# Optimization experiments

Measured on AMD Instinct MI355X. Metric: run time of the kernel, lower is better.

## Reference

```python
import jax, jax.numpy as jnp
import numpy as np

HIDDEN = 1024
D_INNER = 2048      # expand * hidden
STATE = 16          # state_dim n
DT_RANK = 64        # ceil(hidden/16)
D_CONV = 4
B, S = 2, 2048
EPS = 1e-5


def setup_inputs() -> dict:
    key = jax.random.key(0)
    ks = jax.random.split(key, 10)
    sc = lambda fan_in: 1.0 / np.sqrt(fan_in)
    x = jax.random.normal(ks[0], (B, S, HIDDEN), dtype=jnp.float32)
    norm_w = jnp.ones((HIDDEN,), dtype=jnp.float32)
    in_proj_w = jax.random.uniform(ks[1], (2 * D_INNER, HIDDEN), minval=-sc(HIDDEN), maxval=sc(HIDDEN), dtype=jnp.float32)
    conv_w = jax.random.uniform(ks[2], (D_INNER, 1, D_CONV), minval=-sc(D_CONV), maxval=sc(D_CONV), dtype=jnp.float32)
    conv_b = jax.random.uniform(ks[3], (D_INNER,), minval=-sc(D_CONV), maxval=sc(D_CONV), dtype=jnp.float32)
    x_proj_w = jax.random.uniform(ks[4], (DT_RANK + 2 * STATE, D_INNER), minval=-sc(D_INNER), maxval=sc(D_INNER), dtype=jnp.float32)
    dt_proj_w = jax.random.uniform(ks[5], (D_INNER, DT_RANK), minval=-sc(DT_RANK), maxval=sc(DT_RANK), dtype=jnp.float32)
    dt_proj_b = jax.random.uniform(ks[6], (D_INNER,), minval=-sc(DT_RANK), maxval=sc(DT_RANK), dtype=jnp.float32)
    A_log = jnp.log(jnp.broadcast_to(jnp.arange(1, STATE + 1, dtype=jnp.float32), (D_INNER, STATE)))
    D = jnp.ones((D_INNER,), dtype=jnp.float32)
    out_proj_w = jax.random.uniform(ks[7], (HIDDEN, D_INNER), minval=-sc(D_INNER), maxval=sc(D_INNER), dtype=jnp.float32)
    return {"x": x, "norm_w": norm_w, "in_proj_w": in_proj_w, "conv_w": conv_w,
            "conv_b": conv_b, "x_proj_w": x_proj_w, "dt_proj_w": dt_proj_w,
            "dt_proj_b": dt_proj_b, "A_log": A_log, "D": D, "out_proj_w": out_proj_w}


def _selective_scan(u, delta, A, Bm, Cm, D):
    # u, delta: [b,s,d]; A: [d,n]; Bm, Cm: [b,s,n]; D: [d]
    deltaA = jnp.exp(jnp.einsum('bsd,dn->bsdn', delta, A))          # [b,s,d,n]
    deltaB_u = jnp.einsum('bsd,bsn,bsd->bsdn', delta, Bm, u)        # [b,s,d,n]

    def step(h, inp):
        dA_t, dBu_t, C_t = inp                                       # [b,d,n],[b,d,n],[b,n]
        h = dA_t * h + dBu_t
        y = jnp.einsum('bdn,bn->bd', h, C_t)
        return h, y

    h0 = jnp.zeros((u.shape[0], u.shape[2], A.shape[1]), dtype=u.dtype)
    _, ys = jax.lax.scan(step, h0,
                         (deltaA.transpose(1, 0, 2, 3),
                          deltaB_u.transpose(1, 0, 2, 3),
                          Cm.transpose(1, 0, 2)))
    y = ys.transpose(1, 0, 2)                                        # [b,s,d]
    return y + u * D


def reference(x, norm_w, in_proj_w, conv_w, conv_b, x_proj_w, dt_proj_w,
              dt_proj_b, A_log, D, out_proj_w):
    # RMSNorm
    xn = x * jax.lax.rsqrt(jnp.mean(x * x, axis=-1, keepdims=True) + EPS) * norm_w

    # in_proj -> split
    x_and_res = xn @ in_proj_w.T                                     # [b,s,2*d_inner]
    xi, res = jnp.split(x_and_res, 2, axis=-1)

    # causal depthwise conv1d (left-pad d_conv-1, truncate to s)
    xc = jax.lax.conv_general_dilated(
        xi.transpose(0, 2, 1), conv_w,
        window_strides=(1,), padding=[(D_CONV - 1, 0)],
        dimension_numbers=('NCH', 'OIH', 'NCH'),
        feature_group_count=D_INNER) + conv_b[None, :, None]
    xc = jax.nn.silu(xc.transpose(0, 2, 1))                          # [b,s,d_inner]

    # ssm
    A = -jnp.exp(A_log)
    x_dbl = xc @ x_proj_w.T                                          # [b,s,dt_rank+2n]
    dt, Bm, Cm = jnp.split(x_dbl, [DT_RANK, DT_RANK + STATE], axis=-1)
    delta = jax.nn.softplus(dt @ dt_proj_w.T + dt_proj_b)            # [b,s,d_inner]
    y = _selective_scan(xc, delta, A, Bm, Cm, D)

    y = y * jax.nn.silu(res)
    out = y @ out_proj_w.T
    return out + x
```

## Files before the change

### kernel.cpp

```cpp
#include <hip/hip_runtime.h>
#include <math.h>

#define HIDDEN   1024
#define D_INNER  2048
#define NSTATE   16
#define DT_RANK  64
#define BATCH    2
#define SEQ      2048
#define T_TOK    (BATCH * SEQ)
#define XDBL     (DT_RANK + 2 * NSTATE)
#define NCH      64
#define CHL      (SEQ / NCH)
#define BDN      (BATCH * D_INNER * NSTATE)

typedef float f32x4   __attribute__((ext_vector_type(4)));
typedef short bf16x8  __attribute__((ext_vector_type(8)));
typedef short short4v __attribute__((ext_vector_type(4)));

#define AS1 __attribute__((address_space(1)))
#define AS3 __attribute__((address_space(3)))
#define GLOAD(src, dst) __builtin_amdgcn_global_load_lds( \
    (const AS1 unsigned int*)(src), (AS3 unsigned int*)(dst), 16, 0, 0)

__device__ __forceinline__ float silu_f(float x) { return x / (1.0f + __expf(-x)); }
__device__ __forceinline__ float softplus_f(float x) {
    return fmaxf(x, 0.0f) + log1pf(__expf(-fabsf(x)));
}
__device__ __forceinline__ unsigned short f2bf(float x) {
    unsigned int u = __float_as_uint(x);
    u += 0x7fffu + ((u >> 16) & 1u);
    return (unsigned short)(u >> 16);
}
__device__ __forceinline__ float bf2f(unsigned short h) {
    return __uint_as_float(((unsigned int)h) << 16);
}

__device__ __forceinline__ void pack_seg(
        const float* __restrict__ w, unsigned short* __restrict__ wp,
        int K, int segs, int i) {
    int kq = K >> 2;
    int row = i / kq;
    int c = (i - row * kq) << 2;
    float4 v = *(const float4*)(w + (size_t)row * K + c);
    short4v hi, lo;
    hi.x = f2bf(v.x); hi.y = f2bf(v.y); hi.z = f2bf(v.z); hi.w = f2bf(v.w);
    lo.x = f2bf(v.x - bf2f(hi.x)); lo.y = f2bf(v.y - bf2f(hi.y));
    lo.z = f2bf(v.z - bf2f(hi.z)); lo.w = f2bf(v.w - bf2f(hi.w));
    size_t b0 = (size_t)row * (segs * K) + c;
    *(short4v*)(wp + b0) = hi;
    if (segs == 2) *(short4v*)(wp + b0 + K) = lo;
}

__global__ __launch_bounds__(256) void wpack_all_kernel(
        const float* __restrict__ win,  unsigned short* __restrict__ pin,
        const float* __restrict__ wout, unsigned short* __restrict__ pout,
        const float* __restrict__ wx,   unsigned short* __restrict__ px,
        const float* __restrict__ wdt,  unsigned short* __restrict__ pdt) {
    int bid = blockIdx.x;
    int t = threadIdx.x;
    if (bid < 4096) {
        pack_seg(win, pin, HIDDEN, 1, bid * 256 + t);
    } else if (bid < 6144) {
        pack_seg(wout, pout, D_INNER, 1, (bid - 4096) * 256 + t);
    } else if (bid < 6336) {
        pack_seg(wx, px, D_INNER, 2, (bid - 6144) * 256 + t);
    } else {
        pack_seg(wdt, pdt, DT_RANK, 2, (bid - 6336) * 256 + t);
    }
}

__global__ __launch_bounds__(256) void rmsnorm_pack_kernel(
        const float* __restrict__ x, const float* __restrict__ w,
        unsigned short* __restrict__ xn_p) {
    int row = blockIdx.x;
    float4 v = ((const float4*)(x + (size_t)row * HIDDEN))[threadIdx.x];
    float ss = v.x*v.x + v.y*v.y + v.z*v.z + v.w*v.w;
    #pragma unroll
    for (int off = 32; off; off >>= 1) ss += __shfl_down(ss, off);
    __shared__ float wsum[4];
    if ((threadIdx.x & 63) == 0) wsum[threadIdx.x >> 6] = ss;
    __syncthreads();
    float scale = rsqrtf((wsum[0] + wsum[1] + wsum[2] + wsum[3]) / (float)HIDDEN + 1e-5f);
    float4 wv = ((const float4*)w)[threadIdx.x];
    float o0 = v.x * scale * wv.x, o1 = v.y * scale * wv.y;
    float o2 = v.z * scale * wv.z, o3 = v.w * scale * wv.w;
    short4v hi, lo;
    hi.x = f2bf(o0); hi.y = f2bf(o1); hi.z = f2bf(o2); hi.w = f2bf(o3);
    lo.x = f2bf(o0 - bf2f(hi.x)); lo.y = f2bf(o1 - bf2f(hi.y));
    lo.z = f2bf(o2 - bf2f(hi.z)); lo.w = f2bf(o3 - bf2f(hi.w));
    size_t b0 = (size_t)row * (2 * HIDDEN) + threadIdx.x * 4;
    *(short4v*)&xn_p[b0]          = hi;
    *(short4v*)&xn_p[b0 + HIDDEN] = lo;
}

template<int EPI>
__global__ __launch_bounds__(256, 2) void mgemm2_kernel(
        const unsigned short* __restrict__ Ap, int Asr, int loOff,
        const unsigned short* __restrict__ Wp, int Wsr,
        int klen, float* __restrict__ C0, float* __restrict__ C1,
        int ldout, size_t partStride) {
    __shared__ short Ah[128 * 64];
    __shared__ short Al[128 * 64];
    __shared__ short Bh[256 * 64];
    const int t = threadIdx.x;
    const int w = t >> 6, l = t & 63;
    const int m0 = blockIdx.y * 128, n0 = blockIdx.x * 256;
    const int kbeg = blockIdx.z * klen;
    const int lrow = l & 15;
    f32x4 acc[8][4];
    #pragma unroll
    for (int m = 0; m < 8; ++m)
        #pragma unroll
        for (int n = 0; n < 4; ++n) {
            acc[m][n].x = 0.f; acc[m][n].y = 0.f; acc[m][n].z = 0.f; acc[m][n].w = 0.f;
        }
    const int srow8 = l >> 3;
    const int sc8   = (l & 7) ^ srow8;
    const unsigned short* ga = Ap + (size_t)(m0 + w * 32 + srow8) * Asr + sc8 * 8;
    const unsigned short* gb = Wp + (size_t)(n0 + w * 64 + srow8) * Wsr + sc8 * 8;
    for (int k0 = kbeg; k0 < kbeg + klen; k0 += 64) {
        __syncthreads();
        #pragma unroll
        for (int q = 0; q < 4; ++q) {
            const int ar = (w * 32 + q * 8) * 128;
            GLOAD(ga + k0 + (size_t)q * 8 * Asr,         (char*)Ah + ar);
            GLOAD(ga + loOff + k0 + (size_t)q * 8 * Asr, (char*)Al + ar);
        }
        #pragma unroll
        for (int q = 0; q < 8; ++q)
            GLOAD(gb + k0 + (size_t)q * 8 * Wsr, (char*)Bh + (w * 64 + q * 8) * 128);
        __syncthreads();
        #pragma unroll
        for (int kk = 0; kk < 2; ++kk) {
            const int slot = ((kk * 4 + (l >> 4)) ^ (l & 7)) * 8;
            bf16x8 bh[4];
            #pragma unroll
            for (int n = 0; n < 4; ++n)
                bh[n] = *(const bf16x8*)&Bh[(w * 64 + n * 16 + lrow) * 64 + slot];
            #pragma unroll
            for (int m = 0; m < 8; ++m) {
                bf16x8 ah = *(const bf16x8*)&Ah[(m * 16 + lrow) * 64 + slot];
                bf16x8 al = *(const bf16x8*)&Al[(m * 16 + lrow) * 64 + slot];
                #pragma unroll
                for (int n = 0; n < 4; ++n) {
                    acc[m][n] = __builtin_amdgcn_mfma_f32_16x16x32_bf16(
                        ah, bh[n], acc[m][n], 0, 0, 0);
                    acc[m][n] = __builtin_amdgcn_mfma_f32_16x16x32_bf16(
                        al, bh[n], acc[m][n], 0, 0, 0);
                }
            }
        }
    }
    float* dst;
    int cbase;
    if (EPI == 0) {
        dst   = (n0 < D_INNER) ? C0 : C1;
        cbase = (n0 < D_INNER) ? n0 : n0 - D_INNER;
    } else {
        dst   = C0 + blockIdx.z * partStride;
        cbase = n0;
    }
    #pragma unroll
    for (int m = 0; m < 8; ++m) {
        #pragma unroll
        for (int n = 0; n < 4; ++n) {
            #pragma unroll
            for (int j = 0; j < 4; ++j) {
                int row = m0 + m * 16 + (l >> 4) * 4 + j;
                int col = cbase + w * 64 + n * 16 + (l & 15);
                dst[(size_t)row * ldout + col] = acc[m][n][j];
            }
        }
    }
}

template<int EPI>
__global__ __launch_bounds__(256) void mgemm_kernel(
        const unsigned short* __restrict__ Ap, const unsigned short* __restrict__ Wp,
        int Klog, int klen, int brows, float* __restrict__ C0,
        int ldout, size_t partStride, const float* __restrict__ bias) {
    __shared__ short lds[4 * 128 * 64];
    short* Ah = lds;
    short* Al = lds + 128 * 64;
    short* Bh = lds + 2 * 128 * 64;
    short* Bl = lds + 3 * 128 * 64;
    const int t = threadIdx.x;
    const int w = t >> 6, l = t & 63;
    const int m0 = blockIdx.y * 128, n0 = blockIdx.x * 128;
    const int kbeg = blockIdx.z * klen;
    const int wr = (w >> 1) * 64, wc = (w & 1) * 64;
    const int lrow = l & 15;
    f32x4 acc[4][4];
    #pragma unroll
    for (int m = 0; m < 4; ++m)
        #pragma unroll
        for (int n = 0; n < 4; ++n) {
            acc[m][n].x = 0.f; acc[m][n].y = 0.f; acc[m][n].z = 0.f; acc[m][n].w = 0.f;
        }
    const int Asr = 2 * Klog;
    const int Wsr = 2 * Klog;
    const int srow = w * 32 + (l >> 3);
    const int sc8  = (l & 7) ^ ((l >> 3) & 7);
    const int brow = min(n0 + srow, brows - 1);
    const unsigned short* ga = Ap + (size_t)(m0 + srow) * Asr + sc8 * 8;
    const unsigned short* gb = Wp + (size_t)brow * Wsr + sc8 * 8;
    for (int k0 = kbeg; k0 < kbeg + klen; k0 += 64) {
        __syncthreads();
        #pragma unroll
        for (int q = 0; q < 4; ++q) {
            const int doff = (w * 32 + q * 8) * 128;
            GLOAD(ga + k0 + (size_t)q * 8 * Asr,        (char*)Ah + doff);
            GLOAD(ga + Klog + k0 + (size_t)q * 8 * Asr, (char*)Al + doff);
            GLOAD(gb + k0 + (size_t)q * 8 * Wsr,        (char*)Bh + doff);
            GLOAD(gb + Klog + k0 + (size_t)q * 8 * Wsr, (char*)Bl + doff);
        }
        __syncthreads();
        #pragma unroll
        for (int kk = 0; kk < 2; ++kk) {
            const int slot = ((kk * 4 + (l >> 4)) ^ (l & 7)) * 8;
            bf16x8 ah[4], al[4], bh[4], bl[4];
            #pragma unroll
            for (int m = 0; m < 4; ++m) {
                ah[m] = *(const bf16x8*)&Ah[(wr + m * 16 + lrow) * 64 + slot];
                al[m] = *(const bf16x8*)&Al[(wr + m * 16 + lrow) * 64 + slot];
            }
            #pragma unroll
            for (int n = 0; n < 4; ++n) {
                bh[n] = *(const bf16x8*)&Bh[(wc + n * 16 + lrow) * 64 + slot];
                bl[n] = *(const bf16x8*)&Bl[(wc + n * 16 + lrow) * 64 + slot];
            }
            #pragma unroll
            for (int m = 0; m < 4; ++m)
                #pragma unroll
                for (int n = 0; n < 4; ++n) {
                    acc[m][n] = __builtin_amdgcn_mfma_f32_16x16x32_bf16(
                        ah[m], bh[n], acc[m][n], 0, 0, 0);
                    acc[m][n] = __builtin_amdgcn_mfma_f32_16x16x32_bf16(
                        al[m], bh[n], acc[m][n], 0, 0, 0);
                    acc[m][n] = __builtin_amdgcn_mfma_f32_16x16x32_bf16(
                        ah[m], bl[n], acc[m][n], 0, 0, 0);
                }
        }
    }
    float* dst = (EPI == 2) ? (C0 + blockIdx.z * partStride) : C0;
    #pragma unroll
    for (int m = 0; m < 4; ++m) {
        #pragma unroll
        for (int n = 0; n < 4; ++n) {
            #pragma unroll
            for (int j = 0; j < 4; ++j) {
                int row = m0 + wr + m * 16 + (l >> 4) * 4 + j;
                int col = n0 + wc + n * 16 + (l & 15);
                float v = acc[m][n][j];
                if (EPI == 2) {
                    dst[(size_t)row * ldout + col] = v;
                } else {
                    C0[(size_t)row * ldout + col] = softplus_f(v + bias[col]);
                }
            }
        }
    }
}

__global__ __launch_bounds__(256) void reduce4_kernel(
        const float* __restrict__ parts, size_t partStride,
        const float* __restrict__ x, float* __restrict__ out) {
    size_t i = (size_t)blockIdx.x * 256 + threadIdx.x;
    float4 a = ((const float4*)(parts))[i];
    float4 b = ((const float4*)(parts + partStride))[i];
    float4 c = ((const float4*)(parts + 2 * partStride))[i];
    float4 d = ((const float4*)(parts + 3 * partStride))[i];
    float4 xv = ((const float4*)x)[i];
    float4 o;
    o.x = a.x + b.x + c.x + d.x + xv.x;
    o.y = a.y + b.y + c.y + d.y + xv.y;
    o.z = a.z + b.z + c.z + d.z + xv.z;
    o.w = a.w + b.w + c.w + d.w + xv.w;
    ((float4*)out)[i] = o;
}

__global__ __launch_bounds__(256) void reduceX_kernel(
        const float* __restrict__ parts, float* __restrict__ xdbl,
        unsigned short* __restrict__ dtp) {
    int i = blockIdx.x * 256 + threadIdx.x;
    int row = i / 24;
    int c = (i - row * 24) * 4;
    float4 s = make_float4(0.f, 0.f, 0.f, 0.f);
    #pragma unroll
    for (int z = 0; z < 8; ++z) {
        float4 a = *(const float4*)(parts + (size_t)z * 524288 + (size_t)row * 128 + c);
        s.x += a.x; s.y += a.y; s.z += a.z; s.w += a.w;
    }
    *(float4*)(xdbl + (size_t)row * XDBL + c) = s;
    if (c < DT_RANK) {
        short4v hi, lo;
        hi.x = f2bf(s.x); hi.y = f2bf(s.y); hi.z = f2bf(s.z); hi.w = f2bf(s.w);
        lo.x = f2bf(s.x - bf2f(hi.x)); lo.y = f2bf(s.y - bf2f(hi.y));
        lo.z = f2bf(s.z - bf2f(hi.z)); lo.w = f2bf(s.w - bf2f(hi.w));
        size_t b0 = (size_t)row * 128 + c;
        *(short4v*)(dtp + b0)      = hi;
        *(short4v*)(dtp + b0 + 64) = lo;
    }
}

__global__ __launch_bounds__(256) void conv_silu_kernel(
        const float* __restrict__ xi, const float* __restrict__ w,
        const float* __restrict__ b, unsigned short* __restrict__ xc_p) {
    size_t i = (size_t)blockIdx.x * 256 + threadIdx.x;
    int d = (int)(i & (D_INNER - 1));
    int tt = (int)(i >> 11);
    int s = tt & (SEQ - 1);
    float4 wv = ((const float4*)w)[d];
    float acc = b[d];
    if (s >= 3) acc += wv.x * xi[i - 3 * D_INNER];
    if (s >= 2) acc += wv.y * xi[i - 2 * D_INNER];
    if (s >= 1) acc += wv.z * xi[i - 1 * D_INNER];
    acc += wv.w * xi[i];
    float o = silu_f(acc);
    unsigned short hi = f2bf(o);
    unsigned short lo = f2bf(o - bf2f(hi));
    size_t o2 = (size_t)tt * (2 * D_INNER) + d;
    xc_p[o2]           = hi;
    xc_p[o2 + D_INNER] = lo;
}


__global__ __launch_bounds__(256) void scanA_kernel(
        const unsigned short* __restrict__ xcp, const float* __restrict__ delta,
        const float* __restrict__ xdbl, const float* __restrict__ A_log,
        float* __restrict__ hpart, float* __restrict__ Pp) {
    __shared__ float sB[CHL * NSTATE];
    const int bid = blockIdx.x;
    const int b    = bid >> 9;
    const int c    = (bid >> 3) & 63;
    const int dblk = bid & 7;
    const int d    = (dblk << 8) + threadIdx.x;
    const int rowbase = b * SEQ + c * CHL;
    #pragma unroll
    for (int q = 0; q < 2; ++q) {
        int e = threadIdx.x + q * 256;
        int r = e >> 4, n = e & 15;
        sB[e] = xdbl[(size_t)(rowbase + r) * XDBL + DT_RANK + n];
    }
    float adn[NSTATE];
    #pragma unroll
    for (int k = 0; k < 4; ++k) {
        float4 a = *(const float4*)(A_log + d * NSTATE + k * 4);
        adn[k*4+0] = -__expf(a.x); adn[k*4+1] = -__expf(a.y);
        adn[k*4+2] = -__expf(a.z); adn[k*4+3] = -__expf(a.w);
    }
    float h[NSTATE], P[NSTATE];
    #pragma unroll
    for (int n = 0; n < NSTATE; ++n) { h[n] = 0.f; P[n] = 1.f; }
    __syncthreads();
    #pragma unroll 4
    for (int r = 0; r < CHL; ++r) {
        const int row = rowbase + r;
        const float* brow = &sB[r * NSTATE];
        size_t o2 = (size_t)row * (2 * D_INNER) + d;
        float dl = delta[(size_t)row * D_INNER + d];
        float u  = bf2f(xcp[o2]) + bf2f(xcp[o2 + D_INNER]);
        float du = dl * u;
        #pragma unroll
        for (int n = 0; n < NSTATE; ++n) {
            float dA = __expf(dl * adn[n]);
            h[n] = fmaf(dA, h[n], du * brow[n]);
            P[n] *= dA;
        }
    }
    size_t base = (size_t)c * BDN + (size_t)(b * D_INNER + d) * NSTATE;
    #pragma unroll
    for (int k = 0; k < 4; ++k) {
        *(float4*)(hpart + base + k * 4) = make_float4(h[k*4], h[k*4+1], h[k*4+2], h[k*4+3]);
        *(float4*)(Pp    + base + k * 4) = make_float4(P[k*4], P[k*4+1], P[k*4+2], P[k*4+3]);
    }
}

__global__ __launch_bounds__(256) void scanB_kernel(
        float* __restrict__ hpart, const float* __restrict__ Pp) {
    int idx = blockIdx.x * 256 + threadIdx.x;
    float h = 0.f;
    for (int c = 0; c < NCH; ++c) {
        size_t o = (size_t)c * BDN + idx;
        float hp = hpart[o];
        float p  = Pp[o];
        hpart[o] = h;
        h = fmaf(p, h, hp);
    }
}

__global__ __launch_bounds__(256) void scanC_kernel(
        const unsigned short* xcp, const float* __restrict__ delta,
        const float* __restrict__ xdbl, const float* __restrict__ A_log,
        const float* __restrict__ Dp, const float* __restrict__ hstart,
        const float* __restrict__ res, unsigned short* y_p) {
    __shared__ float sB[CHL * NSTATE];
    __shared__ float sC[CHL * NSTATE];
    const int bid = blockIdx.x;
    const int b    = bid >> 9;
    const int c    = (bid >> 3) & 63;
    const int dblk = bid & 7;
    const int d    = (dblk << 8) + threadIdx.x;
    const int rowbase = b * SEQ + c * CHL;
    #pragma unroll
    for (int q = 0; q < 2; ++q) {
        int e = threadIdx.x + q * 256;
        int r = e >> 4, n = e & 15;
        sB[e] = xdbl[(size_t)(rowbase + r) * XDBL + DT_RANK + n];
        sC[e] = xdbl[(size_t)(rowbase + r) * XDBL + DT_RANK + NSTATE + n];
    }
    float adn[NSTATE];
    #pragma unroll
    for (int k = 0; k < 4; ++k) {
        float4 a = *(const float4*)(A_log + d * NSTATE + k * 4);
        adn[k*4+0] = -__expf(a.x); adn[k*4+1] = -__expf(a.y);
        adn[k*4+2] = -__expf(a.z); adn[k*4+3] = -__expf(a.w);
    }
    const float Dd = Dp[d];
    float h[NSTATE];
    size_t base = (size_t)c * BDN + (size_t)(b * D_INNER + d) * NSTATE;
    #pragma unroll
    for (int k = 0; k < 4; ++k) {
        float4 hv = *(const float4*)(hstart + base + k * 4);
        h[k*4] = hv.x; h[k*4+1] = hv.y; h[k*4+2] = hv.z; h[k*4+3] = hv.w;
    }
    __syncthreads();
    #pragma unroll 4
    for (int r = 0; r < CHL; ++r) {
        const int row = rowbase + r;
        const float* brow = &sB[r * NSTATE];
        const float* crow = &sC[r * NSTATE];
        size_t o2 = (size_t)row * (2 * D_INNER) + d;
        float dl = delta[(size_t)row * D_INNER + d];
        float u  = bf2f(xcp[o2]) + bf2f(xcp[o2 + D_INNER]);
        float du = dl * u;
        float ys[4];
        ys[0] = u * Dd; ys[1] = 0.f; ys[2] = 0.f; ys[3] = 0.f;
        #pragma unroll
        for (int n = 0; n < NSTATE; ++n) {
            float dA = __expf(dl * adn[n]);
            h[n] = fmaf(dA, h[n], du * brow[n]);
            ys[n & 3] = fmaf(h[n], crow[n], ys[n & 3]);
        }
        float ysum = (ys[0] + ys[1]) + (ys[2] + ys[3]);
        float rv = res[(size_t)row * D_INNER + d];
        float gv = ysum * silu_f(rv);
        unsigned short hi = f2bf(gv);
        unsigned short lo = f2bf(gv - bf2f(hi));
        y_p[o2]           = hi;
        y_p[o2 + D_INNER] = lo;
    }
}

extern "C" void kernel_launch(void* const* d_in, const int* in_sizes, int n_in,
                              void* d_out, int out_size, void* d_ws, size_t ws_size,
                              hipStream_t stream) {
    const float* x         = (const float*)d_in[0];
    const float* norm_w    = (const float*)d_in[1];
    const float* in_proj_w = (const float*)d_in[2];
    const float* conv_w    = (const float*)d_in[3];
    const float* conv_b    = (const float*)d_in[4];
    const float* x_proj_w  = (const float*)d_in[5];
    const float* dt_proj_w = (const float*)d_in[6];
    const float* dt_proj_b = (const float*)d_in[7];
    const float* A_log     = (const float*)d_in[8];
    const float* Dp        = (const float*)d_in[9];
    const float* out_proj_w= (const float*)d_in[10];
    float* out = (float*)d_out;
    float* ws  = (float*)d_ws;

    const size_t M8 = (size_t)T_TOK * D_INNER;
    float* res   = ws;
    float* delta = res + M8;
    float* xdbl  = delta + M8;
    unsigned short* xn_p   = (unsigned short*)(xdbl + (size_t)T_TOK * XDBL);
    unsigned short* w_in_p = xn_p   + (size_t)4096 * 2048;
    unsigned short* w_out_p= w_in_p + (size_t)4096 * 1024;
    unsigned short* w_xp_p = w_out_p+ (size_t)1024 * 2048;
    unsigned short* w_dt_p = w_xp_p + (size_t)96 * 4096;
    unsigned short* xc_p   = w_dt_p + (size_t)2048 * 128;
    unsigned short* dtp_p  = xc_p   + (size_t)4096 * 4096;
    float* xi    = (float*)(dtp_p + (size_t)4096 * 128);
    float* hpart = xi;
    float* Pp    = xi + (size_t)BDN * NCH;
    float* parts_x = delta;
    unsigned short* y_p = xc_p;
    float* parts = ws;
    const size_t partStride = (size_t)T_TOK * HIDDEN;

    wpack_all_kernel<<<6464, 256, 0, stream>>>(in_proj_w, w_in_p, out_proj_w, w_out_p,
                                               x_proj_w, w_xp_p, dt_proj_w, w_dt_p);

    rmsnorm_pack_kernel<<<T_TOK, 256, 0, stream>>>(x, norm_w, xn_p);

    {
        dim3 g(4096 / 256, T_TOK / 128, 1);
        mgemm2_kernel<0><<<g, 256, 0, stream>>>(xn_p, 2 * HIDDEN, HIDDEN,
                                                w_in_p, HIDDEN, HIDDEN,
                                                xi, res, D_INNER, 0);
    }

    conv_silu_kernel<<<(int)(M8 / 256), 256, 0, stream>>>(xi, conv_w, conv_b, xc_p);

    {
        dim3 g(1, T_TOK / 128, 8);
        mgemm_kernel<2><<<g, 256, 0, stream>>>(xc_p, w_xp_p, D_INNER, D_INNER / 8,
                                               96, parts_x, 128, 524288, nullptr);
    }
    reduceX_kernel<<<T_TOK * 24 / 256, 256, 0, stream>>>(parts_x, xdbl, dtp_p);

    {
        dim3 g(D_INNER / 128, T_TOK / 128, 1);
        mgemm_kernel<3><<<g, 256, 0, stream>>>(dtp_p, w_dt_p, DT_RANK, DT_RANK,
                                               D_INNER, delta, D_INNER, 0, dt_proj_b);
    }

    scanA_kernel<<<BATCH * NCH * 8, 256, 0, stream>>>(xc_p, delta, xdbl, A_log, hpart, Pp);
    scanB_kernel<<<BDN / 256, 256, 0, stream>>>(hpart, Pp);
    scanC_kernel<<<BATCH * NCH * 8, 256, 0, stream>>>(xc_p, delta, xdbl, A_log, Dp,
                                                      hpart, res, y_p);

    {
        dim3 g(HIDDEN / 256, T_TOK / 128, 4);
        mgemm2_kernel<2><<<g, 256, 0, stream>>>(y_p, 2 * D_INNER, D_INNER,
                                                w_out_p, D_INNER, D_INNER / 4,
                                                parts, nullptr, HIDDEN, partStride);
    }
    reduce4_kernel<<<(int)(partStride / 4 / 256), 256, 0, stream>>>(parts, partStride, x, out);
}
```

Baseline: 295.6 us.

## Store GEMM outputs as bf16 pairs and fuse rmsnorm into weight-pack kernel

The in_proj GEMM now writes xi as a packed bf16 hi/lo pair and res as a single bf16. The out_proj split-K partials are stored as bf16 instead of fp32, and the conv, scan and reduce kernels read these narrower formats. The rmsnorm is folded into the weight-packing launch as extra blocks, which saves one kernel launch. The aim is to halve intermediate memory traffic, at the cost of bf16 rounding on res and on the output partials, which may reduce accuracy.

After: 287.8 us. -2.6%, faster.

```diff
diff --git a/kernel.cpp b/kernel.cpp
--- a/kernel.cpp
+++ b/kernel.cpp
@@ -51,11 +51,13 @@
     if (segs == 2) *(short4v*)(wp + b0 + K) = lo;
 }
 
-__global__ __launch_bounds__(256) void wpack_all_kernel(
+__global__ __launch_bounds__(256) void wpack_rms_kernel(
         const float* __restrict__ win,  unsigned short* __restrict__ pin,
         const float* __restrict__ wout, unsigned short* __restrict__ pout,
         const float* __restrict__ wx,   unsigned short* __restrict__ px,
-        const float* __restrict__ wdt,  unsigned short* __restrict__ pdt) {
+        const float* __restrict__ wdt,  unsigned short* __restrict__ pdt,
+        const float* __restrict__ x,    const float* __restrict__ nw,
+        unsigned short* __restrict__ xn_p) {
     int bid = blockIdx.x;
     int t = threadIdx.x;
     if (bid < 4096) {
@@ -64,40 +66,36 @@
         pack_seg(wout, pout, D_INNER, 1, (bid - 4096) * 256 + t);
     } else if (bid < 6336) {
         pack_seg(wx, px, D_INNER, 2, (bid - 6144) * 256 + t);
+    } else if (bid < 6464) {
+        pack_seg(wdt, pdt, DT_RANK, 2, (bid - 6336) * 256 + t);
     } else {
-        pack_seg(wdt, pdt, DT_RANK, 2, (bid - 6336) * 256 + t);
-    }
-}
-
-__global__ __launch_bounds__(256) void rmsnorm_pack_kernel(
-        const float* __restrict__ x, const float* __restrict__ w,
-        unsigned short* __restrict__ xn_p) {
-    int row = blockIdx.x;
-    float4 v = ((const float4*)(x + (size_t)row * HIDDEN))[threadIdx.x];
-    float ss = v.x*v.x + v.y*v.y + v.z*v.z + v.w*v.w;
-    #pragma unroll
-    for (int off = 32; off; off >>= 1) ss += __shfl_down(ss, off);
-    __shared__ float wsum[4];
-    if ((threadIdx.x & 63) == 0) wsum[threadIdx.x >> 6] = ss;
-    __syncthreads();
-    float scale = rsqrtf((wsum[0] + wsum[1] + wsum[2] + wsum[3]) / (float)HIDDEN + 1e-5f);
-    float4 wv = ((const float4*)w)[threadIdx.x];
-    float o0 = v.x * scale * wv.x, o1 = v.y * scale * wv.y;
-    float o2 = v.z * scale * wv.z, o3 = v.w * scale * wv.w;
-    short4v hi, lo;
-    hi.x = f2bf(o0); hi.y = f2bf(o1); hi.z = f2bf(o2); hi.w = f2bf(o3);
-    lo.x = f2bf(o0 - bf2f(hi.x)); lo.y = f2bf(o1 - bf2f(hi.y));
-    lo.z = f2bf(o2 - bf2f(hi.z)); lo.w = f2bf(o3 - bf2f(hi.w));
-    size_t b0 = (size_t)row * (2 * HIDDEN) + threadIdx.x * 4;
-    *(short4v*)&xn_p[b0]          = hi;
-    *(short4v*)&xn_p[b0 + HIDDEN] = lo;
+        int row = bid - 6464;
+        float4 v = ((const float4*)(x + (size_t)row * HIDDEN))[t];
+        float ss = v.x*v.x + v.y*v.y + v.z*v.z + v.w*v.w;
+        #pragma unroll
+        for (int off = 32; off; off >>= 1) ss += __shfl_down(ss, off);
+        __shared__ float wsum[4];
+        if ((t & 63) == 0) wsum[t >> 6] = ss;
+        __syncthreads();
+        float scale = rsqrtf((wsum[0] + wsum[1] + wsum[2] + wsum[3]) / (float)HIDDEN + 1e-5f);
+        float4 wv = ((const float4*)nw)[t];
+        float o0 = v.x * scale * wv.x, o1 = v.y * scale * wv.y;
+        float o2 = v.z * scale * wv.z, o3 = v.w * scale * wv.w;
+        short4v hi, lo;
+        hi.x = f2bf(o0); hi.y = f2bf(o1); hi.z = f2bf(o2); hi.w = f2bf(o3);
+        lo.x = f2bf(o0 - bf2f(hi.x)); lo.y = f2bf(o1 - bf2f(hi.y));
+        lo.z = f2bf(o2 - bf2f(hi.z)); lo.w = f2bf(o3 - bf2f(hi.w));
+        size_t b0 = (size_t)row * (2 * HIDDEN) + t * 4;
+        *(short4v*)&xn_p[b0]          = hi;
+        *(short4v*)&xn_p[b0 + HIDDEN] = lo;
+    }
 }
 
 template<int EPI>
 __global__ __launch_bounds__(256, 2) void mgemm2_kernel(
         const unsigned short* __restrict__ Ap, int Asr, int loOff,
         const unsigned short* __restrict__ Wp, int Wsr,
-        int klen, float* __restrict__ C0, float* __restrict__ C1,
+        int klen, unsigned short* __restrict__ O0, unsigned short* __restrict__ O1,
         int ldout, size_t partStride) {
     __shared__ short Ah[128 * 64];
     __shared__ short Al[128 * 64];
@@ -151,15 +149,6 @@
             }
         }
     }
-    float* dst;
-    int cbase;
-    if (EPI == 0) {
-        dst   = (n0 < D_INNER) ? C0 : C1;
-        cbase = (n0 < D_INNER) ? n0 : n0 - D_INNER;
-    } else {
-        dst   = C0 + blockIdx.z * partStride;
-        cbase = n0;
-    }
     #pragma unroll
     for (int m = 0; m < 8; ++m) {
         #pragma unroll
@@ -167,8 +156,21 @@
             #pragma unroll
             for (int j = 0; j < 4; ++j) {
                 int row = m0 + m * 16 + (l >> 4) * 4 + j;
-                int col = cbase + w * 64 + n * 16 + (l & 15);
-                dst[(size_t)row * ldout + col] = acc[m][n][j];
+                int col = n0 + w * 64 + n * 16 + (l & 15);
+                float v = acc[m][n][j];
+                if (EPI == 0) {
+                    if (col < D_INNER) {
+                        unsigned short hi = f2bf(v);
+                        unsigned short lo = f2bf(v - bf2f(hi));
+                        size_t o = (size_t)row * (2 * D_INNER) + col;
+                        O0[o]           = hi;
+                        O0[o + D_INNER] = lo;
+                    } else {
+                        O1[(size_t)row * D_INNER + (col - D_INNER)] = f2bf(v);
+                    }
+                } else {
+                    O0[blockIdx.z * partStride + (size_t)row * ldout + col] = f2bf(v);
+                }
             }
         }
     }
@@ -263,19 +265,19 @@
 }
 
 __global__ __launch_bounds__(256) void reduce4_kernel(
-        const float* __restrict__ parts, size_t partStride,
+        const unsigned short* __restrict__ parts, size_t partStride,
         const float* __restrict__ x, float* __restrict__ out) {
     size_t i = (size_t)blockIdx.x * 256 + threadIdx.x;
-    float4 a = ((const float4*)(parts))[i];
-    float4 b = ((const float4*)(parts + partStride))[i];
-    float4 c = ((const float4*)(parts + 2 * partStride))[i];
-    float4 d = ((const float4*)(parts + 3 * partStride))[i];
+    short4v a = *(const short4v*)(parts + i * 4);
+    short4v b = *(const short4v*)(parts + partStride + i * 4);
+    short4v c = *(const short4v*)(parts + 2 * partStride + i * 4);
+    short4v d = *(const short4v*)(parts + 3 * partStride + i * 4);
     float4 xv = ((const float4*)x)[i];
     float4 o;
-    o.x = a.x + b.x + c.x + d.x + xv.x;
-    o.y = a.y + b.y + c.y + d.y + xv.y;
-    o.z = a.z + b.z + c.z + d.z + xv.z;
-    o.w = a.w + b.w + c.w + d.w + xv.w;
+    o.x = bf2f(a.x) + bf2f(b.x) + bf2f(c.x) + bf2f(d.x) + xv.x;
+    o.y = bf2f(a.y) + bf2f(b.y) + bf2f(c.y) + bf2f(d.y) + xv.y;
+    o.z = bf2f(a.z) + bf2f(b.z) + bf2f(c.z) + bf2f(d.z) + xv.z;
+    o.w = bf2f(a.w) + bf2f(b.w) + bf2f(c.w) + bf2f(d.w) + xv.w;
     ((float4*)out)[i] = o;
 }
 
@@ -304,7 +306,7 @@
 }
 
 __global__ __launch_bounds__(256) void conv_silu_kernel(
-        const float* __restrict__ xi, const float* __restrict__ w,
+        const unsigned short* __restrict__ xi_p, const float* __restrict__ w,
         const float* __restrict__ b, unsigned short* __restrict__ xc_p) {
     size_t i = (size_t)blockIdx.x * 256 + threadIdx.x;
     int d = (int)(i & (D_INNER - 1));
@@ -312,10 +314,19 @@
     int s = tt & (SEQ - 1);
     float4 wv = ((const float4*)w)[d];
     float acc = b[d];
-    if (s >= 3) acc += wv.x * xi[i - 3 * D_INNER];
-    if (s >= 2) acc += wv.y * xi[i - 2 * D_INNER];
-    if (s >= 1) acc += wv.z * xi[i - 1 * D_INNER];
-    acc += wv.w * xi[i];
+    #pragma unroll
+    for (int k = 3; k >= 1; --k) {
+        if (s >= k) {
+            size_t o = (size_t)(tt - k) * (2 * D_INNER) + d;
+            float u = bf2f(xi_p[o]) + bf2f(xi_p[o + D_INNER]);
+            acc += ((const float*)&wv)[3 - k] * u;
+        }
+    }
+    {
+        size_t o = (size_t)tt * (2 * D_INNER) + d;
+        float u = bf2f(xi_p[o]) + bf2f(xi_p[o + D_INNER]);
+        acc += wv.w * u;
+    }
     float o = silu_f(acc);
     unsigned short hi = f2bf(o);
     unsigned short lo = f2bf(o - bf2f(hi));
@@ -393,7 +404,7 @@
         const unsigned short* xcp, const float* __restrict__ delta,
         const float* __restrict__ xdbl, const float* __restrict__ A_log,
         const float* __restrict__ Dp, const float* __restrict__ hstart,
-        const float* __restrict__ res, unsigned short* y_p) {
+        const unsigned short* __restrict__ res_b, unsigned short* y_p) {
     __shared__ float sB[CHL * NSTATE];
     __shared__ float sC[CHL * NSTATE];
     const int bid = blockIdx.x;
@@ -443,7 +454,7 @@
             ys[n & 3] = fmaf(h[n], crow[n], ys[n & 3]);
         }
         float ysum = (ys[0] + ys[1]) + (ys[2] + ys[3]);
-        float rv = res[(size_t)row * D_INNER + d];
+        float rv = bf2f(res_b[(size_t)row * D_INNER + d]);
         float gv = ysum * silu_f(rv);
         unsigned short hi = f2bf(gv);
         unsigned short lo = f2bf(gv - bf2f(hi));
@@ -470,8 +481,9 @@
     float* ws  = (float*)d_ws;
 
     const size_t M8 = (size_t)T_TOK * D_INNER;
-    float* res   = ws;
-    float* delta = res + M8;
+    unsigned short* res_b  = (unsigned short*)ws;
+    unsigned short* parts_b= (unsigned short*)ws;
+    float* delta = ws + M8;
     float* xdbl  = delta + M8;
     unsigned short* xn_p   = (unsigned short*)(xdbl + (size_t)T_TOK * XDBL);
     unsigned short* w_in_p = xn_p   + (size_t)4096 * 2048;
@@ -480,27 +492,25 @@
     unsigned short* w_dt_p = w_xp_p + (size_t)96 * 4096;
     unsigned short* xc_p   = w_dt_p + (size_t)2048 * 128;
     unsigned short* dtp_p  = xc_p   + (size_t)4096 * 4096;
-    float* xi    = (float*)(dtp_p + (size_t)4096 * 128);
-    float* hpart = xi;
-    float* Pp    = xi + (size_t)BDN * NCH;
+    unsigned short* xi_p   = dtp_p + (size_t)4096 * 128;
+    float* hpart = (float*)xi_p;
+    float* Pp    = hpart + (size_t)BDN * NCH;
     float* parts_x = delta;
     unsigned short* y_p = xc_p;
-    float* parts = ws;
     const size_t partStride = (size_t)T_TOK * HIDDEN;
 
-    wpack_all_kernel<<<6464, 256, 0, stream>>>(in_proj_w, w_in_p, out_proj_w, w_out_p,
-                                               x_proj_w, w_xp_p, dt_proj_w, w_dt_p);
-
-    rmsnorm_pack_kernel<<<T_TOK, 256, 0, stream>>>(x, norm_w, xn_p);
+    wpack_rms_kernel<<<6464 + T_TOK, 256, 0, stream>>>(
+        in_proj_w, w_in_p, out_proj_w, w_out_p, x_proj_w, w_xp_p,
+        dt_proj_w, w_dt_p, x, norm_w, xn_p);
 
     {
         dim3 g(4096 / 256, T_TOK / 128, 1);
         mgemm2_kernel<0><<<g, 256, 0, stream>>>(xn_p, 2 * HIDDEN, HIDDEN,
                                                 w_in_p, HIDDEN, HIDDEN,
-                                                xi, res, D_INNER, 0);
-    }
-
-    conv_silu_kernel<<<(int)(M8 / 256), 256, 0, stream>>>(xi, conv_w, conv_b, xc_p);
+                                                xi_p, res_b, 0, 0);
+    }
+
+    conv_silu_kernel<<<(int)(M8 / 256), 256, 0, stream>>>(xi_p, conv_w, conv_b, xc_p);
 
     {
         dim3 g(1, T_TOK / 128, 8);
@@ -518,13 +528,13 @@
     scanA_kernel<<<BATCH * NCH * 8, 256, 0, stream>>>(xc_p, delta, xdbl, A_log, hpart, Pp);
     scanB_kernel<<<BDN / 256, 256, 0, stream>>>(hpart, Pp);
     scanC_kernel<<<BATCH * NCH * 8, 256, 0, stream>>>(xc_p, delta, xdbl, A_log, Dp,
-                                                      hpart, res, y_p);
+                                                      hpart, res_b, y_p);
 
     {
         dim3 g(HIDDEN / 256, T_TOK / 128, 4);
         mgemm2_kernel<2><<<g, 256, 0, stream>>>(y_p, 2 * D_INNER, D_INNER,
                                                 w_out_p, D_INNER, D_INNER / 4,
-                                                parts, nullptr, HIDDEN, partStride);
-    }
-    reduce4_kernel<<<(int)(partStride / 4 / 256), 256, 0, stream>>>(parts, partStride, x, out);
-}
+                                                parts_b, nullptr, HIDDEN, partStride);
+    }
+    reduce4_kernel<<<(int)(partStride / 4 / 256), 256, 0, stream>>>(parts_b, partStride, x, out);
+}
```
